# Kernel tuning notes

Measured on AMD Instinct MI355X. Metric: run time of the kernel, lower is better.

## Reference

```python
import jax, jax.numpy as jnp
import numpy as np

K = 3   # up_kernel
S = 2   # scale_factor per stage
COMP = 64  # compressed channels (mmcv CARAFEPack default)


def _conv2d(x, w, b, pad):
    y = jax.lax.conv_general_dilated(
        x, w, window_strides=(1, 1), padding=[(pad, pad), (pad, pad)],
        dimension_numbers=('NCHW', 'OIHW', 'NCHW'))
    return y + b[None, :, None, None]


def _carafe_stage(x, wc, bc, we, be):
    B, C, H, W = x.shape
    # kernel prediction branch
    comp = _conv2d(x, wc, bc, 0)                 # [B, 64, H, W]
    m = _conv2d(comp, we, be, 1)                 # [B, K*K*S*S, H, W]
    # pixel shuffle: [B, K*K, S, S, H, W] -> [B, K*K, H, S, W, S]
    m = m.reshape(B, K * K, S, S, H, W).transpose(0, 1, 4, 2, 5, 3)
    # softmax over the K*K kernel weights per output pixel
    m = jax.nn.softmax(m, axis=1)                # [B, 9, H, S, W, S]
    # 3x3 neighborhoods of source (row-major kernel order, matching mmcv)
    xp = jnp.pad(x, ((0, 0), (0, 0), (1, 1), (1, 1)))
    patches = jnp.stack(
        [xp[:, :, dy:dy + H, dx:dx + W] for dy in range(K) for dx in range(K)],
        axis=2)                                   # [B, C, 9, H, W]
    # content-aware reassembly: weights shared across channels (up_group=1)
    out = jnp.einsum('bckhw,bkhpwq->bchpwq', patches, m)
    return out.reshape(B, C, S * H, S * W)


def setup_inputs() -> dict:
    key = jax.random.key(0)
    ks = jax.random.split(key, 12)
    B, C, H, W = 2, 256, 16, 16
    inp = {
        'source': jax.random.normal(ks[0], (B, C, H, W), jnp.float32),
        'guidance': jax.random.normal(ks[1], (B, 3, 256, 256), jnp.float32),
    }
    sc = 1.0 / np.sqrt(C)        # fan-in of 1x1 compressor
    se = 1.0 / np.sqrt(COMP * K * K)  # fan-in of 3x3 encoder
    for i in range(4):
        inp[f'wc{i+1}'] = jax.random.normal(ks[2 + 2 * i], (COMP, C, 1, 1), jnp.float32) * sc
        inp[f'bc{i+1}'] = jnp.zeros((COMP,), jnp.float32)
        inp[f'we{i+1}'] = jax.random.normal(ks[3 + 2 * i], (K * K * S * S, COMP, K, K), jnp.float32) * se
        inp[f'be{i+1}'] = jnp.zeros((K * K * S * S,), jnp.float32)
    return inp


def reference(source, guidance,
              wc1, bc1, we1, be1,
              wc2, bc2, we2, be2,
              wc3, bc3, we3, be3,
              wc4, bc4, we4, be4):
    x = _carafe_stage(source, wc1, bc1, we1, be1)
    x = _carafe_stage(x, wc2, bc2, we2, be2)
    x = _carafe_stage(x, wc3, bc3, we3, be3)
    x = _carafe_stage(x, wc4, bc4, we4, be4)
    return x
```

## Files before the change

kernel.cpp:

```cpp
#include <hip/hip_runtime.h>

#define LB __launch_bounds__(256)

__global__ LB void prep_weights(
    const float* __restrict__ wcA, const float* __restrict__ wcB,
    const float* __restrict__ wcC, const float* __restrict__ wcD,
    const float* __restrict__ weA, const float* __restrict__ weB,
    const float* __restrict__ weC, const float* __restrict__ weD,
    float* __restrict__ wcT, float* __restrict__ weT)
{
    int seg = blockIdx.y;
    int t = blockIdx.x * 256 + threadIdx.x;
    if (seg < 4) {
        if (t >= 64 * 256) return;
        const float* w = (seg == 0) ? wcA : (seg == 1) ? wcB : (seg == 2) ? wcC : wcD;
        int c = t & 255, o = t >> 8;
        wcT[seg * 16384 + c * 64 + o] = w[t];
    } else {
        if (t >= 36 * 64 * 9) return;
        const float* w = (seg == 4) ? weA : (seg == 5) ? weB : (seg == 6) ? weC : weD;
        int kt = t % 9;
        int r = t / 9;
        int i = r & 63;
        int o = r >> 6;
        int kk = o >> 2, pq = o & 3;
        weT[(seg - 4) * 20736 + ((pq * 64 + i) * 9 + kt) * 9 + kk] = w[t];
    }
}

__global__ LB void compress_k(const float* __restrict__ x, const float* __restrict__ wcT,
                              const float* __restrict__ bc, float* __restrict__ comp, int lgW)
{
    int lane = threadIdx.x & 63;
    int og = __builtin_amdgcn_readfirstlane(threadIdx.x >> 6);
    int lgHW = 2 * lgW;
    int HW = 1 << lgHW;
    int pix = blockIdx.x * 64 + lane;
    int b = pix >> lgHW;
    int hw = pix & (HW - 1);
    const float* xp = x + ((size_t)b << lgHW) * 256 + hw;
    float acc[16];
    const float* bp = bc + og * 16;
    #pragma unroll
    for (int j = 0; j < 16; j++) acc[j] = bp[j];
    const float* wr = wcT + og * 16;
    #pragma unroll 4
    for (int c = 0; c < 256; c++) {
        float xv = xp[(size_t)c << lgHW];
        #pragma unroll
        for (int j = 0; j < 16; j++) acc[j] += wr[c * 64 + j] * xv;
    }
    float* op = comp + ((size_t)b * 64 + og * 16) * HW + hw;
    #pragma unroll
    for (int j = 0; j < 16; j++) op[(size_t)j << lgHW] = acc[j];
}

__global__ LB void encoder_k(const float* __restrict__ comp, const float* __restrict__ weT,
                             const float* __restrict__ be, float* __restrict__ mnorm, int lgW)
{
    int lgHW = 2 * lgW;
    int HW = 1 << lgHW, W = 1 << lgW, H = W;
    int idx = blockIdx.x * 256 + threadIdx.x;
    int pq = __builtin_amdgcn_readfirstlane(idx >> (lgHW + 1));
    int pix = idx & (2 * HW - 1);
    int b = pix >> lgHW;
    int hw = pix & (HW - 1);
    int h = hw >> lgW, w = hw & (W - 1);

    int off[9];
    float msk[9];
    #pragma unroll
    for (int ky = 0; ky < 3; ky++) {
        int ys = h + ky - 1;
        bool yok = (unsigned)ys < (unsigned)H;
        #pragma unroll
        for (int kx = 0; kx < 3; kx++) {
            int xs = w + kx - 1;
            bool ok = yok && ((unsigned)xs < (unsigned)W);
            int kt = ky * 3 + kx;
            off[kt] = ok ? ((ys << lgW) + xs) : 0;
            msk[kt] = ok ? 1.f : 0.f;
        }
    }
    float acc[9];
    #pragma unroll
    for (int kk = 0; kk < 9; kk++) acc[kk] = be[kk * 4 + pq];
    const float* wp = weT + pq * 576 * 9;
    const float* cb = comp + (size_t)b * 64 * HW;
    for (int i = 0; i < 64; i++) {
        const float* ci = cb + ((size_t)i << lgHW);
        #pragma unroll
        for (int kt = 0; kt < 9; kt++) {
            float cv = ci[off[kt]] * msk[kt];
            const float* wt = wp + (i * 9 + kt) * 9;
            #pragma unroll
            for (int kk = 0; kk < 9; kk++) acc[kk] += wt[kk] * cv;
        }
    }
    float m = acc[0];
    #pragma unroll
    for (int kk = 1; kk < 9; kk++) m = fmaxf(m, acc[kk]);
    float s = 0.f;
    #pragma unroll
    for (int kk = 0; kk < 9; kk++) { acc[kk] = __expf(acc[kk] - m); s += acc[kk]; }
    float r = 1.f / s;
    float* mp = mnorm + (size_t)b * 36 * HW + hw;
    #pragma unroll
    for (int kk = 0; kk < 9; kk++) mp[(size_t)(kk * 4 + pq) << lgHW] = acc[kk] * r;
}

__global__ LB void reassembly_k(const float* __restrict__ x, const float* __restrict__ mnorm,
                                float* __restrict__ out, int lgW)
{
    int lgHW = 2 * lgW;
    int HW = 1 << lgHW, W = 1 << lgW, H = W;
    int lane = threadIdx.x & 63;
    int cg = threadIdx.x >> 6;
    int nbsh = lgHW - 5;
    int pb = blockIdx.x & ((1 << nbsh) - 1);
    int cs = blockIdx.x >> nbsh;
    int pix = pb * 64 + lane;
    int b = pix >> lgHW;
    int hw = pix & (HW - 1);
    int h = hw >> lgW, w = hw & (W - 1);

    int off[9];
    float msk[9];
    #pragma unroll
    for (int ky = 0; ky < 3; ky++) {
        int ys = h + ky - 1;
        bool yok = (unsigned)ys < (unsigned)H;
        #pragma unroll
        for (int kx = 0; kx < 3; kx++) {
            int xs = w + kx - 1;
            bool ok = yok && ((unsigned)xs < (unsigned)W);
            int kt = ky * 3 + kx;
            off[kt] = ok ? ((ys << lgW) + xs) : 0;
            msk[kt] = ok ? 1.f : 0.f;
        }
    }
    const float* mp = mnorm + (size_t)b * 36 * HW + hw;
    float wreg[36];
    #pragma unroll
    for (int ch = 0; ch < 36; ch++) wreg[ch] = mp[(size_t)ch << lgHW];

    int c0 = (cs * 4 + cg) * 16;
    const float* xb = x + ((size_t)b * 256 + c0) * HW;
    size_t OW = (size_t)W * 2;
    float* ob = out + (((size_t)b * 256 + c0) * 2 * H + 2 * h) * OW + 2 * w;
    for (int it = 0; it < 16; it++) {
        const float* xc = xb + ((size_t)it << lgHW);
        float a00 = 0.f, a01 = 0.f, a10 = 0.f, a11 = 0.f;
        #pragma unroll
        for (int kt = 0; kt < 9; kt++) {
            float tap = xc[off[kt]] * msk[kt];
            a00 += tap * wreg[kt * 4 + 0];
            a01 += tap * wreg[kt * 4 + 1];
            a10 += tap * wreg[kt * 4 + 2];
            a11 += tap * wreg[kt * 4 + 3];
        }
        float* oc = ob + (size_t)it * 2 * H * OW;
        *(float2*)oc = make_float2(a00, a01);
        *(float2*)(oc + OW) = make_float2(a10, a11);
    }
}

extern "C" void kernel_launch(void* const* d_in, const int* in_sizes, int n_in,
                              void* d_out, int out_size, void* d_ws, size_t ws_size,
                              hipStream_t stream)
{
    const float* src = (const float*)d_in[0];
    const float* wc[4]; const float* bc[4]; const float* we[4]; const float* be[4];
    for (int s = 0; s < 4; s++) {
        wc[s] = (const float*)d_in[2 + 4 * s];
        bc[s] = (const float*)d_in[3 + 4 * s];
        we[s] = (const float*)d_in[4 + 4 * s];
        be[s] = (const float*)d_in[5 + 4 * s];
    }
    float* ws   = (float*)d_ws;
    float* x1   = ws;
    float* x2   = x1 + 524288;
    float* x3   = x2 + 2097152;
    float* comp = x3 + 8388608;
    float* mn   = comp + 2097152;
    float* wcT  = mn + 1179648;
    float* weT  = wcT + 65536;

    prep_weights<<<dim3(81, 8), 256, 0, stream>>>(
        wc[0], wc[1], wc[2], wc[3], we[0], we[1], we[2], we[3], wcT, weT);

    const float* xin = src;
    float* stage_out[4] = {x1, x2, x3, (float*)d_out};
    int lgW = 4;
    for (int s = 0; s < 4; s++) {
        int HW = 1 << (2 * lgW);
        int nb = HW >> 5;
        compress_k<<<nb, 256, 0, stream>>>(xin, wcT + s * 16384, bc[s], comp, lgW);
        encoder_k<<<nb, 256, 0, stream>>>(comp, weT + s * 20736, be[s], mn, lgW);
        reassembly_k<<<nb * 4, 256, 0, stream>>>(xin, mn, stage_out[s], lgW);
        xin = stage_out[s];
        lgW++;
    }
}
```

Before: 519.2 us.

## Re-partition compress and reassembly work and vectorize encoder weight loads

The compressor now splits its 64 output channels into 8 groups on grid.y, with 8 outputs per thread. On the larger stages each thread handles two pixels, read and written as float2, and the weights are laid out as [group][c][8] to match. Encoder weights are padded to 16 per tap so each tap's 9 weights load as two float4s plus one scalar, and the 9 taps are gathered before the FMA chain. Reassembly uses 4 channels per thread on the two small stages to launch more blocks, which should raise occupancy. The trade-off is that each source pixel is now read by 8 channel groups instead of 4, which leans more on cache, and the padded weight buffer takes more workspace.

```diff
diff --git a/kernel.cpp b/kernel.cpp
--- a/kernel.cpp
+++ b/kernel.cpp
@@ -15,7 +15,7 @@
         if (t >= 64 * 256) return;
         const float* w = (seg == 0) ? wcA : (seg == 1) ? wcB : (seg == 2) ? wcC : wcD;
         int c = t & 255, o = t >> 8;
-        wcT[seg * 16384 + c * 64 + o] = w[t];
+        wcT[seg * 16384 + ((o >> 3) * 256 + c) * 8 + (o & 7)] = w[t];
     } else {
         if (t >= 36 * 64 * 9) return;
         const float* w = (seg == 4) ? weA : (seg == 5) ? weB : (seg == 6) ? weC : weD;
@@ -24,42 +24,66 @@
         int i = r & 63;
         int o = r >> 6;
         int kk = o >> 2, pq = o & 3;
-        weT[(seg - 4) * 20736 + ((pq * 64 + i) * 9 + kt) * 9 + kk] = w[t];
-    }
-}
-
+        weT[(seg - 4) * 36864 + ((pq * 64 + i) * 9 + kt) * 16 + kk] = w[t];
+    }
+}
+
+template<int PPT>
 __global__ LB void compress_k(const float* __restrict__ x, const float* __restrict__ wcT,
                               const float* __restrict__ bc, float* __restrict__ comp, int lgW)
 {
-    int lane = threadIdx.x & 63;
-    int og = __builtin_amdgcn_readfirstlane(threadIdx.x >> 6);
-    int lgHW = 2 * lgW;
-    int HW = 1 << lgHW;
-    int pix = blockIdx.x * 64 + lane;
+    const int lgHW = 2 * lgW;
+    const int HW = 1 << lgHW;
+    const int og = blockIdx.y;
+    int tid = blockIdx.x * 256 + threadIdx.x;
+    int pix = tid * PPT;
     int b = pix >> lgHW;
     int hw = pix & (HW - 1);
-    const float* xp = x + ((size_t)b << lgHW) * 256 + hw;
-    float acc[16];
-    const float* bp = bc + og * 16;
-    #pragma unroll
-    for (int j = 0; j < 16; j++) acc[j] = bp[j];
-    const float* wr = wcT + og * 16;
+    const float* xp = x + (((size_t)b * 256) << lgHW) + hw;
+    const float* wr = wcT + og * 2048;
+
+    float acc[8][PPT];
+    #pragma unroll
+    for (int j = 0; j < 8; j++) {
+        float bv = bc[og * 8 + j];
+        #pragma unroll
+        for (int p = 0; p < PPT; p++) acc[j][p] = bv;
+    }
+
     #pragma unroll 4
     for (int c = 0; c < 256; c++) {
-        float xv = xp[(size_t)c << lgHW];
-        #pragma unroll
-        for (int j = 0; j < 16; j++) acc[j] += wr[c * 64 + j] * xv;
-    }
-    float* op = comp + ((size_t)b * 64 + og * 16) * HW + hw;
-    #pragma unroll
-    for (int j = 0; j < 16; j++) op[(size_t)j << lgHW] = acc[j];
+        float xv[PPT];
+        if (PPT == 1) {
+            xv[0] = xp[(size_t)c << lgHW];
+        } else {
+            float2 t2 = *(const float2*)(xp + ((size_t)c << lgHW));
+            xv[0] = t2.x; xv[1] = t2.y;
+        }
+        const float* w8 = wr + c * 8;
+        #pragma unroll
+        for (int j = 0; j < 8; j++) {
+            float wv = w8[j];
+            #pragma unroll
+            for (int p = 0; p < PPT; p++) acc[j][p] += wv * xv[p];
+        }
+    }
+
+    float* op = comp + (((size_t)b * 64 + og * 8) << lgHW) + hw;
+    #pragma unroll
+    for (int j = 0; j < 8; j++) {
+        if (PPT == 1) {
+            op[(size_t)j << lgHW] = acc[j][0];
+        } else {
+            *(float2*)(op + ((size_t)j << lgHW)) = make_float2(acc[j][0], acc[j][1]);
+        }
+    }
 }
 
 __global__ LB void encoder_k(const float* __restrict__ comp, const float* __restrict__ weT,
                              const float* __restrict__ be, float* __restrict__ mnorm, int lgW)
 {
-    int lgHW = 2 * lgW;
-    int HW = 1 << lgHW, W = 1 << lgW, H = W;
+    const int lgHW = 2 * lgW;
+    const int HW = 1 << lgHW, W = 1 << lgW, H = W;
     int idx = blockIdx.x * 256 + threadIdx.x;
     int pq = __builtin_amdgcn_readfirstlane(idx >> (lgHW + 1));
     int pix = idx & (2 * HW - 1);
@@ -82,21 +106,33 @@
             msk[kt] = ok ? 1.f : 0.f;
         }
     }
+
     float acc[9];
     #pragma unroll
     for (int kk = 0; kk < 9; kk++) acc[kk] = be[kk * 4 + pq];
-    const float* wp = weT + pq * 576 * 9;
-    const float* cb = comp + (size_t)b * 64 * HW;
+
+    const float* wp = weT + pq * 9216;
+    const float* cb = comp + (((size_t)b) << lgHW) * 64;
+    #pragma unroll 2
     for (int i = 0; i < 64; i++) {
         const float* ci = cb + ((size_t)i << lgHW);
+        float tap[9];
+        #pragma unroll
+        for (int kt = 0; kt < 9; kt++) tap[kt] = ci[off[kt]] * msk[kt];
+        const float* wi = wp + i * 144;
         #pragma unroll
         for (int kt = 0; kt < 9; kt++) {
-            float cv = ci[off[kt]] * msk[kt];
-            const float* wt = wp + (i * 9 + kt) * 9;
-            #pragma unroll
-            for (int kk = 0; kk < 9; kk++) acc[kk] += wt[kk] * cv;
-        }
-    }
+            const float* wt = wi + kt * 16;
+            float4 w0 = *(const float4*)(wt);
+            float4 w1 = *(const float4*)(wt + 4);
+            float  w8 = wt[8];
+            float tv = tap[kt];
+            acc[0] += w0.x * tv; acc[1] += w0.y * tv; acc[2] += w0.z * tv;
+            acc[3] += w0.w * tv; acc[4] += w1.x * tv; acc[5] += w1.y * tv;
+            acc[6] += w1.z * tv; acc[7] += w1.w * tv; acc[8] += w8 * tv;
+        }
+    }
+
     float m = acc[0];
     #pragma unroll
     for (int kk = 1; kk < 9; kk++) m = fmaxf(m, acc[kk]);
@@ -104,16 +140,17 @@
     #pragma unroll
     for (int kk = 0; kk < 9; kk++) { acc[kk] = __expf(acc[kk] - m); s += acc[kk]; }
     float r = 1.f / s;
-    float* mp = mnorm + (size_t)b * 36 * HW + hw;
+    float* mp = mnorm + (((size_t)b * 36) << lgHW) + hw;
     #pragma unroll
     for (int kk = 0; kk < 9; kk++) mp[(size_t)(kk * 4 + pq) << lgHW] = acc[kk] * r;
 }
 
+template<int CPT>
 __global__ LB void reassembly_k(const float* __restrict__ x, const float* __restrict__ mnorm,
                                 float* __restrict__ out, int lgW)
 {
-    int lgHW = 2 * lgW;
-    int HW = 1 << lgHW, W = 1 << lgW, H = W;
+    const int lgHW = 2 * lgW;
+    const int HW = 1 << lgHW, W = 1 << lgW, H = W;
     int lane = threadIdx.x & 63;
     int cg = threadIdx.x >> 6;
     int nbsh = lgHW - 5;
@@ -139,16 +176,17 @@
             msk[kt] = ok ? 1.f : 0.f;
         }
     }
-    const float* mp = mnorm + (size_t)b * 36 * HW + hw;
+    const float* mp = mnorm + (((size_t)b * 36) << lgHW) + hw;
     float wreg[36];
     #pragma unroll
     for (int ch = 0; ch < 36; ch++) wreg[ch] = mp[(size_t)ch << lgHW];
 
-    int c0 = (cs * 4 + cg) * 16;
+    int c0 = (cs * 4 + cg) * CPT;
     const float* xb = x + ((size_t)b * 256 + c0) * HW;
     size_t OW = (size_t)W * 2;
     float* ob = out + (((size_t)b * 256 + c0) * 2 * H + 2 * h) * OW + 2 * w;
-    for (int it = 0; it < 16; it++) {
+    #pragma unroll 2
+    for (int it = 0; it < CPT; it++) {
         const float* xc = xb + ((size_t)it << lgHW);
         float a00 = 0.f, a01 = 0.f, a10 = 0.f, a11 = 0.f;
         #pragma unroll
@@ -194,10 +232,19 @@
     int lgW = 4;
     for (int s = 0; s < 4; s++) {
         int HW = 1 << (2 * lgW);
-        int nb = HW >> 5;
-        compress_k<<<nb, 256, 0, stream>>>(xin, wcT + s * 16384, bc[s], comp, lgW);
-        encoder_k<<<nb, 256, 0, stream>>>(comp, weT + s * 20736, be[s], mn, lgW);
-        reassembly_k<<<nb * 4, 256, 0, stream>>>(xin, mn, stage_out[s], lgW);
+        int npix = 2 * HW;
+        if (s < 2)
+            compress_k<1><<<dim3(npix / 256, 8), 256, 0, stream>>>(
+                xin, wcT + s * 16384, bc[s], comp, lgW);
+        else
+            compress_k<2><<<dim3(npix / 512, 8), 256, 0, stream>>>(
+                xin, wcT + s * 16384, bc[s], comp, lgW);
+        encoder_k<<<npix >> 6, 256, 0, stream>>>(comp, weT + s * 36864, be[s], mn, lgW);
+        int nb = npix >> 6;
+        if (s < 2)
+            reassembly_k<4><<<nb * 16, 256, 0, stream>>>(xin, mn, stage_out[s], lgW);
+        else
+            reassembly_k<16><<<nb * 4, 256, 0, stream>>>(xin, mn, stage_out[s], lgW);
         xin = stage_out[s];
         lgW++;
     }
```

New measurement: 534.1 us. 1.03x slower.
